# Optimization experiments

Measured on AMD Instinct MI355X. Metric: run time of the kernel, lower is better.

Reference implementation:

```python
import jax, jax.numpy as jnp
import numpy as np

NEG_INF = -1e30  # fp32-safe sentinel for masked max


def setup_inputs() -> dict:
    key = jax.random.key(0)
    ks = jax.random.split(key, 8)
    E = 65536          # num_edge
    S = 1              # neg_samples
    D = 200            # dim_in_time + dim_in_node
    H = 100            # hardcoded hidden width of src_fc/dst_fc
    T = 8              # num edge types
    C = 1              # predict_class
    scale = 1.0 / np.sqrt(D)
    return {
        "h": jax.random.normal(ks[0], (E * (S + 2), D), dtype=jnp.float32),
        "src_W": jax.random.normal(ks[1], (T, D, H), dtype=jnp.float32) * scale,
        "src_b": jax.random.normal(ks[2], (T, H), dtype=jnp.float32) * 0.01,
        "dst_W": jax.random.normal(ks[3], (T, D, H), dtype=jnp.float32) * scale,
        "dst_b": jax.random.normal(ks[4], (T, H), dtype=jnp.float32) * 0.01,
        "out_W": jax.random.normal(ks[5], (T, H, C), dtype=jnp.float32) * (1.0 / np.sqrt(H)),
        "out_b": jax.random.normal(ks[6], (T, C), dtype=jnp.float32) * 0.01,
        "poss_edgetypes": jax.random.randint(ks[7], (E * (1 + S), T), 0, 2, dtype=jnp.int32),
        "neg_samples": S,
    }


def _masked_max_pred(h_s, h_d, mask, src_W, src_b, dst_W, dst_b, out_W, out_b):
    # h_s, h_d: [N, D]; mask: [N, T] bool
    src_enc = jnp.einsum('nd,tdh->nth', h_s, src_W) + src_b      # [N, T, H]
    dst_enc = jnp.einsum('nd,tdh->nth', h_d, dst_W) + dst_b      # [N, T, H]
    hid = jax.nn.relu(src_enc + dst_enc)                          # [N, T, H]
    pred = jnp.einsum('nth,thc->ntc', hid, out_W) + out_b        # [N, T, C]
    masked = jnp.where(mask[:, :, None], pred, NEG_INF)
    best = jnp.max(masked, axis=1)                                # [N, C]
    any_valid = jnp.any(mask, axis=1, keepdims=True)
    return jnp.where(any_valid, best, 0.0)                        # zeros if no valid type


def reference(h, src_W, src_b, dst_W, dst_b, out_W, out_b, poss_edgetypes, neg_samples):
    E = h.shape[0] // (neg_samples + 2)
    h_src = h[:E]
    h_pos_dst = h[E:2 * E]
    h_neg_dst = h[2 * E:]                                         # [S*E, D], neg-major order
    mask = poss_edgetypes.astype(bool)
    pos_mask = mask[:E]
    neg_mask = mask[E:]
    pos_pred = _masked_max_pred(h_src, h_pos_dst, pos_mask,
                                src_W, src_b, dst_W, dst_b, out_W, out_b)
    h_src_tiled = jnp.tile(h_src, (neg_samples, 1))               # matches global_neg_idx = src + neg*E
    neg_pred = _masked_max_pred(h_src_tiled, h_neg_dst, neg_mask,
                                src_W, src_b, dst_W, dst_b, out_W, out_b)
    return pos_pred, neg_pred
```

## Files before the change

### kernel.cpp

```cpp
#include <hip/hip_runtime.h>
#include <stdint.h>


typedef float f32x4 __attribute__((ext_vector_type(4)));
typedef short s16x8 __attribute__((ext_vector_type(8)));

static constexpr int E_NODES  = 65536;
static constexpr int D_DIM    = 200;
static constexpr int H_DIM    = 100;
static constexpr int T_TYPES  = 8;
static constexpr int NPAD     = 112;
static constexpr int NT       = 7;
static constexpr int NSLAB    = 7;
static constexpr int P_TILE   = 128;
static constexpr int THREADS  = 256;
static constexpr int RS_TOTAL = T_TYPES * NSLAB;
static constexpr int SLAB_BYTES = NPAD * 64 * 2;
static constexpr int SLAB_XFERS = SLAB_BYTES / 16;

__device__ unsigned short g_Wt[RS_TOTAL * NPAD * 64];
__device__ float g_bias[T_TYPES * NPAD];
__device__ float g_outw[T_TYPES * NPAD];
__device__ float g_outb[T_TYPES];

__device__ __forceinline__ unsigned short f2bf(float f) {
  unsigned int u = __float_as_uint(f);
  u += 0x7FFFu + ((u >> 16) & 1u);
  return (unsigned short)(u >> 16);
}

__global__ void prep_weights(const float* __restrict__ srcW, const float* __restrict__ dstW,
                             const float* __restrict__ srcB, const float* __restrict__ dstB,
                             const float* __restrict__ outW, const float* __restrict__ outB) {
  int idx = blockIdx.x * blockDim.x + threadIdx.x;
  const int total = RS_TOTAL * NPAD * 64;
  if (idx < total) {
    int kk   = idx & 63;
    int j    = (idx >> 6) % NPAD;
    int rs   = (idx >> 6) / NPAD;
    int slab = rs % NSLAB;
    int t    = rs / NSLAB;
    int k    = slab * 64 + kk;
    float v = 0.0f;
    if (j < H_DIM) {
      if (k < D_DIM)                          v = srcW[(t * D_DIM + k) * H_DIM + j];
      else if (k >= 224 && k < 224 + D_DIM)   v = dstW[(t * D_DIM + (k - 224)) * H_DIM + j];
    }
    int kks = kk ^ ((j & 7) << 3);
    g_Wt[(rs * NPAD + j) * 64 + kks] = f2bf(v);
  }
  if (idx < T_TYPES * NPAD) {
    int t = idx / NPAD, j = idx % NPAD;
    float bb = 0.0f, ww = 0.0f;
    if (j < H_DIM) {
      bb = srcB[t * H_DIM + j] + dstB[t * H_DIM + j];
      ww = outW[t * H_DIM + j];
    }
    g_bias[idx] = bb;
    g_outw[idx] = ww;
    if (j == 0) g_outb[t] = outB[t];
  }
}

__device__ __forceinline__ void stage_B(int rs, unsigned short* dst, int tid) {
  char* src = (char*)g_Wt + (size_t)rs * SLAB_BYTES;
#pragma unroll
  for (int i = 0; i < 4; ++i) {
    int idx = i * THREADS + tid;
    if (idx < SLAB_XFERS) {
      __builtin_amdgcn_global_load_lds(
          (const __attribute__((address_space(1))) void*)(src + idx * 16),
          (__attribute__((address_space(3))) void*)(dst + idx * 8),
          16, 0, 0);
    }
  }
}

__global__ __launch_bounds__(THREADS, 2)
void fused_pred(const float* __restrict__ h, const int* __restrict__ poss,
                float* __restrict__ out) {
  __shared__ __align__(16) unsigned short ldsB[2][NPAD * 64];
  __shared__ __align__(16) int ldsMask[P_TILE * T_TYPES];

  const int tid  = threadIdx.x;
  const int lane = tid & 63;
  const int w    = tid >> 6;
  const int c    = lane & 15;
  const int g    = lane >> 4;
  const int P0   = (int)blockIdx.x * P_TILE;

  {
    const int4* mp = (const int4*)(poss + (size_t)P0 * T_TYPES);
    ((int4*)ldsMask)[tid] = mp[tid];
  }

  stage_B(0, ldsB[0], tid);

  s16x8 A[2][14];
#pragma unroll
  for (int mt = 0; mt < 2; ++mt) {
    const int row = w * 32 + mt * 16 + c;
    const int p   = P0 + row;
    const float* sp = h + (size_t)(p & (E_NODES - 1)) * D_DIM;
    const float* dp = h + ((size_t)E_NODES + (size_t)p) * D_DIM;
#pragma unroll
    for (int ks = 0; ks < 14; ++ks) {
      const float* base = (ks < 7) ? sp : dp;
      const int k0 = ((ks < 7) ? ks : (ks - 7)) * 32 + g * 8;
      s16x8 a = {};
      const bool valid = !((ks == 6 || ks == 13) && (g != 0));
      if (valid) {
        float4 f0 = *(const float4*)(base + k0);
        float4 f1 = *(const float4*)(base + k0 + 4);
        a[0] = (short)f2bf(f0.x); a[1] = (short)f2bf(f0.y);
        a[2] = (short)f2bf(f0.z); a[3] = (short)f2bf(f0.w);
        a[4] = (short)f2bf(f1.x); a[5] = (short)f2bf(f1.y);
        a[6] = (short)f2bf(f1.z); a[7] = (short)f2bf(f1.w);
      }
      A[mt][ks] = a;
    }
  }

  const f32x4 ZERO4 = {0.f, 0.f, 0.f, 0.f};
  f32x4 acc[2][NT];
#pragma unroll
  for (int mt = 0; mt < 2; ++mt)
#pragma unroll
    for (int nt = 0; nt < NT; ++nt) acc[mt][nt] = ZERO4;

  float runmax[2][4];
#pragma unroll
  for (int mt = 0; mt < 2; ++mt)
#pragma unroll
    for (int r = 0; r < 4; ++r) runmax[mt][r] = -1e30f;

  __syncthreads();

  int buf = 0;
  const int swz = (c & 7) << 4;
  for (int t = 0; t < T_TYPES; ++t) {
#pragma unroll
    for (int slab = 0; slab < NSLAB; ++slab) {
      const int s = t * NSLAB + slab;
      if (s + 1 < RS_TOTAL) stage_B(s + 1, ldsB[buf ^ 1], tid);

      const char* B = (const char*)ldsB[buf];
#pragma unroll
      for (int ksl = 0; ksl < 2; ++ksl) {
        const int koff = (ksl * 64 + g * 16) ^ swz;
        const s16x8 a0 = A[0][slab * 2 + ksl];
        const s16x8 a1 = A[1][slab * 2 + ksl];
#pragma unroll
        for (int nt = 0; nt < NT; ++nt) {
          s16x8 b = *(const s16x8*)(B + (nt * 16 + c) * 128 + koff);
          acc[0][nt] = __builtin_amdgcn_mfma_f32_16x16x32_bf16(a0, b, acc[0][nt], 0, 0, 0);
          acc[1][nt] = __builtin_amdgcn_mfma_f32_16x16x32_bf16(a1, b, acc[1][nt], 0, 0, 0);
        }
      }

      if (slab == NSLAB - 1) {
        float bj[NT], wj[NT];
#pragma unroll
        for (int nt = 0; nt < NT; ++nt) {
          const int j = t * NPAD + nt * 16 + c;
          bj[nt] = g_bias[j];
          wj[nt] = g_outw[j];
        }
        const float outb = g_outb[t];
#pragma unroll
        for (int mt = 0; mt < 2; ++mt) {
#pragma unroll
          for (int r = 0; r < 4; ++r) {
            float v = 0.f;
#pragma unroll
            for (int nt = 0; nt < NT; ++nt)
              v += fmaxf(acc[mt][nt][r] + bj[nt], 0.f) * wj[nt];
            v += __shfl_xor(v, 1);
            v += __shfl_xor(v, 2);
            v += __shfl_xor(v, 4);
            v += __shfl_xor(v, 8);
            const float pred = v + outb;
            const int row = w * 32 + mt * 16 + g * 4 + r;
            if (ldsMask[row * T_TYPES + t] != 0)
              runmax[mt][r] = fmaxf(runmax[mt][r], pred);
          }
#pragma unroll
          for (int nt = 0; nt < NT; ++nt) acc[mt][nt] = ZERO4;
        }
      }
      __syncthreads();
      buf ^= 1;
    }
  }

  if (c == 0) {
#pragma unroll
    for (int mt = 0; mt < 2; ++mt)
#pragma unroll
      for (int r = 0; r < 4; ++r) {
        const int row = w * 32 + mt * 16 + g * 4 + r;
        const float v = runmax[mt][r];
        out[P0 + row] = (v > -1e29f) ? v : 0.0f;
      }
  }
}

extern "C" void kernel_launch(void* const* d_in, const int* in_sizes, int n_in,
                              void* d_out, int out_size, void* d_ws, size_t ws_size,
                              hipStream_t stream) {
  const float* h    = (const float*)d_in[0];
  const float* srcW = (const float*)d_in[1];
  const float* srcB = (const float*)d_in[2];
  const float* dstW = (const float*)d_in[3];
  const float* dstB = (const float*)d_in[4];
  const float* outW = (const float*)d_in[5];
  const float* outB = (const float*)d_in[6];
  const int*   poss = (const int*)d_in[7];
  float* out = (float*)d_out;

  const int prep_total = RS_TOTAL * NPAD * 64;
  prep_weights<<<(prep_total + 255) / 256, 256, 0, stream>>>(srcW, dstW, srcB, dstB, outW, outB);

  const int nblocks = (2 * E_NODES) / P_TILE;
  fused_pred<<<nblocks, THREADS, 0, stream>>>(h, poss, out);
}
```

Baseline: 355.9 us.

## Pack K densely into 128-wide slabs, cut K-steps, remap blocks, stage bias in LDS

The weight layout packs the src and dst K ranges contiguously (400 instead of 448 padded), so each type needs 13 MFMA K-steps instead of 14. Weights are staged in 128-wide slabs, which halves the number of barrier-separated stages per type (4 instead of 7). Bias and output weights are now loaded into LDS inside the main kernel instead of a prep pass. The block index is remapped so that pos and neg tiles sharing the same src rows run close together, which should improve L2 reuse. LDS use per block roughly doubles for the B buffers, which may affect occupancy at 2 blocks per CU.

```diff
diff --git a/kernel.cpp b/kernel.cpp
--- a/kernel.cpp
+++ b/kernel.cpp
@@ -5,23 +5,22 @@
 typedef float f32x4 __attribute__((ext_vector_type(4)));
 typedef short s16x8 __attribute__((ext_vector_type(8)));
 
-static constexpr int E_NODES  = 65536;
-static constexpr int D_DIM    = 200;
-static constexpr int H_DIM    = 100;
-static constexpr int T_TYPES  = 8;
-static constexpr int NPAD     = 112;
-static constexpr int NT       = 7;
-static constexpr int NSLAB    = 7;
-static constexpr int P_TILE   = 128;
-static constexpr int THREADS  = 256;
-static constexpr int RS_TOTAL = T_TYPES * NSLAB;
-static constexpr int SLAB_BYTES = NPAD * 64 * 2;
-static constexpr int SLAB_XFERS = SLAB_BYTES / 16;
-
-__device__ unsigned short g_Wt[RS_TOTAL * NPAD * 64];
-__device__ float g_bias[T_TYPES * NPAD];
-__device__ float g_outw[T_TYPES * NPAD];
-__device__ float g_outb[T_TYPES];
+static constexpr int E_NODES = 65536;
+static constexpr int D_DIM   = 200;
+static constexpr int H_DIM   = 100;
+static constexpr int T_TYPES = 8;
+static constexpr int NPAD    = 112;
+static constexpr int NT      = 7;
+static constexpr int KS      = 13;
+static constexpr int BK      = 128;
+static constexpr int SLPT    = 4;
+static constexpr int P_TILE  = 128;
+static constexpr int THREADS = 256;
+static constexpr int N_INT   = T_TYPES * SLPT;
+static constexpr int SLAB_ELEMS = NPAD * BK;
+static constexpr int XFERS_PT   = SLAB_ELEMS * 2 / 16 / THREADS;
+
+__device__ unsigned short g_Wt[N_INT * SLAB_ELEMS];
 
 __device__ __forceinline__ unsigned short f2bf(float f) {
   unsigned int u = __float_as_uint(f);
@@ -29,74 +28,82 @@
   return (unsigned short)(u >> 16);
 }
 
-__global__ void prep_weights(const float* __restrict__ srcW, const float* __restrict__ dstW,
-                             const float* __restrict__ srcB, const float* __restrict__ dstB,
-                             const float* __restrict__ outW, const float* __restrict__ outB) {
+__global__ void prep_weights(const float* __restrict__ srcW, const float* __restrict__ dstW) {
   int idx = blockIdx.x * blockDim.x + threadIdx.x;
-  const int total = RS_TOTAL * NPAD * 64;
-  if (idx < total) {
-    int kk   = idx & 63;
-    int j    = (idx >> 6) % NPAD;
-    int rs   = (idx >> 6) / NPAD;
-    int slab = rs % NSLAB;
-    int t    = rs / NSLAB;
-    int k    = slab * 64 + kk;
-    float v = 0.0f;
-    if (j < H_DIM) {
-      if (k < D_DIM)                          v = srcW[(t * D_DIM + k) * H_DIM + j];
-      else if (k >= 224 && k < 224 + D_DIM)   v = dstW[(t * D_DIM + (k - 224)) * H_DIM + j];
-    }
-    int kks = kk ^ ((j & 7) << 3);
-    g_Wt[(rs * NPAD + j) * 64 + kks] = f2bf(v);
-  }
-  if (idx < T_TYPES * NPAD) {
-    int t = idx / NPAD, j = idx % NPAD;
-    float bb = 0.0f, ww = 0.0f;
-    if (j < H_DIM) {
-      bb = srcB[t * H_DIM + j] + dstB[t * H_DIM + j];
-      ww = outW[t * H_DIM + j];
-    }
-    g_bias[idx] = bb;
-    g_outw[idx] = ww;
-    if (j == 0) g_outb[t] = outB[t];
-  }
-}
-
-__device__ __forceinline__ void stage_B(int rs, unsigned short* dst, int tid) {
-  char* src = (char*)g_Wt + (size_t)rs * SLAB_BYTES;
-#pragma unroll
-  for (int i = 0; i < 4; ++i) {
-    int idx = i * THREADS + tid;
-    if (idx < SLAB_XFERS) {
-      __builtin_amdgcn_global_load_lds(
-          (const __attribute__((address_space(1))) void*)(src + idx * 16),
-          (__attribute__((address_space(3))) void*)(dst + idx * 8),
-          16, 0, 0);
-    }
+  const int total = N_INT * SLAB_ELEMS;
+  if (idx >= total) return;
+  int j   = idx % NPAD;
+  int rem = idx / NPAD;
+  int kk  = rem % BK;
+  int rs  = rem / BK;
+  int sl  = rs & 3;
+  int t   = rs >> 2;
+  int k   = sl * BK + kk;
+  float v = 0.0f;
+  if (j < H_DIM) {
+    if (k < D_DIM)            v = srcW[(t * D_DIM + k) * H_DIM + j];
+    else if (k < 2 * D_DIM)   v = dstW[(t * D_DIM + (k - D_DIM)) * H_DIM + j];
+  }
+  int kks = kk ^ ((j & 7) << 3);
+  g_Wt[(rs * NPAD + j) * BK + kks] = f2bf(v);
+}
+
+__device__ __forceinline__ void stage(int rs, unsigned short* dst, int tid) {
+  const char* src = (const char*)g_Wt + (size_t)rs * SLAB_ELEMS * 2;
+  char* d = (char*)dst;
+#pragma unroll
+  for (int i = 0; i < XFERS_PT; ++i) {
+    const int off = (i * THREADS + tid) * 16;
+    __builtin_amdgcn_global_load_lds(
+        (const __attribute__((address_space(1))) void*)(src + off),
+        (__attribute__((address_space(3))) void*)(d + off),
+        16, 0, 0);
   }
 }
 
 __global__ __launch_bounds__(THREADS, 2)
-void fused_pred(const float* __restrict__ h, const int* __restrict__ poss,
-                float* __restrict__ out) {
-  __shared__ __align__(16) unsigned short ldsB[2][NPAD * 64];
-  __shared__ __align__(16) int ldsMask[P_TILE * T_TYPES];
+void fused_pred(const float* __restrict__ h,
+                const float* __restrict__ srcB, const float* __restrict__ dstB,
+                const float* __restrict__ outW, const float* __restrict__ outB,
+                const int* __restrict__ poss, float* __restrict__ out) {
+  __shared__ __align__(16) unsigned short ldsB[2][SLAB_ELEMS];
+  __shared__ __align__(16) int   ldsMask[P_TILE * T_TYPES];
+  __shared__ float ldsBias[T_TYPES * NPAD];
+  __shared__ float ldsOutw[T_TYPES * NPAD];
+  __shared__ float ldsOutb[T_TYPES];
 
   const int tid  = threadIdx.x;
   const int lane = tid & 63;
   const int w    = tid >> 6;
   const int c    = lane & 15;
   const int g    = lane >> 4;
-  const int P0   = (int)blockIdx.x * P_TILE;
-
-  {
-    const int4* mp = (const int4*)(poss + (size_t)P0 * T_TYPES);
-    ((int4*)ldsMask)[tid] = mp[tid];
-  }
-
-  stage_B(0, ldsB[0], tid);
-
-  s16x8 A[2][14];
+
+  const int l     = ((int)blockIdx.x & 7) * 128 + ((int)blockIdx.x >> 3);
+  const int which = l & 1;
+  const int grp   = l >> 1;
+  const int P0    = which * E_NODES + grp * P_TILE;
+
+  stage(0, ldsB[0], tid);
+  __builtin_amdgcn_sched_barrier(0);
+
+#pragma unroll
+  for (int i = 0; i < 4; ++i) {
+    int idx = i * THREADS + tid;
+    if (idx < T_TYPES * NPAD) {
+      int t = idx / NPAD, j = idx - t * NPAD;
+      float bb = 0.f, ww = 0.f;
+      if (j < H_DIM) {
+        bb = srcB[t * H_DIM + j] + dstB[t * H_DIM + j];
+        ww = outW[t * H_DIM + j];
+      }
+      ldsBias[idx] = bb;
+      ldsOutw[idx] = ww;
+    }
+  }
+  if (tid < T_TYPES) ldsOutb[tid] = outB[tid];
+  ((int4*)ldsMask)[tid] = ((const int4*)(poss + (size_t)P0 * T_TYPES))[tid];
+
+  s16x8 A[2][KS];
 #pragma unroll
   for (int mt = 0; mt < 2; ++mt) {
     const int row = w * 32 + mt * 16 + c;
@@ -104,14 +111,13 @@
     const float* sp = h + (size_t)(p & (E_NODES - 1)) * D_DIM;
     const float* dp = h + ((size_t)E_NODES + (size_t)p) * D_DIM;
 #pragma unroll
-    for (int ks = 0; ks < 14; ++ks) {
-      const float* base = (ks < 7) ? sp : dp;
-      const int k0 = ((ks < 7) ? ks : (ks - 7)) * 32 + g * 8;
+    for (int ks = 0; ks < KS; ++ks) {
+      const int k0 = ks * 32 + g * 8;
       s16x8 a = {};
-      const bool valid = !((ks == 6 || ks == 13) && (g != 0));
-      if (valid) {
-        float4 f0 = *(const float4*)(base + k0);
-        float4 f1 = *(const float4*)(base + k0 + 4);
+      if (k0 < 2 * D_DIM) {
+        const float* base = (k0 < D_DIM) ? (sp + k0) : (dp + (k0 - D_DIM));
+        float4 f0 = *(const float4*)(base);
+        float4 f1 = *(const float4*)(base + 4);
         a[0] = (short)f2bf(f0.x); a[1] = (short)f2bf(f0.y);
         a[2] = (short)f2bf(f0.z); a[3] = (short)f2bf(f0.w);
         a[4] = (short)f2bf(f1.x); a[5] = (short)f2bf(f1.y);
@@ -123,50 +129,51 @@
 
   const f32x4 ZERO4 = {0.f, 0.f, 0.f, 0.f};
   f32x4 acc[2][NT];
-#pragma unroll
-  for (int mt = 0; mt < 2; ++mt)
+  float runmax[2][4];
+#pragma unroll
+  for (int mt = 0; mt < 2; ++mt) {
 #pragma unroll
     for (int nt = 0; nt < NT; ++nt) acc[mt][nt] = ZERO4;
-
-  float runmax[2][4];
-#pragma unroll
-  for (int mt = 0; mt < 2; ++mt)
 #pragma unroll
     for (int r = 0; r < 4; ++r) runmax[mt][r] = -1e30f;
+  }
+
+  const int swz = (c & 7) << 4;
 
   __syncthreads();
 
-  int buf = 0;
-  const int swz = (c & 7) << 4;
   for (int t = 0; t < T_TYPES; ++t) {
 #pragma unroll
-    for (int slab = 0; slab < NSLAB; ++slab) {
-      const int s = t * NSLAB + slab;
-      if (s + 1 < RS_TOTAL) stage_B(s + 1, ldsB[buf ^ 1], tid);
-
-      const char* B = (const char*)ldsB[buf];
-#pragma unroll
-      for (int ksl = 0; ksl < 2; ++ksl) {
-        const int koff = (ksl * 64 + g * 16) ^ swz;
-        const s16x8 a0 = A[0][slab * 2 + ksl];
-        const s16x8 a1 = A[1][slab * 2 + ksl];
+    for (int sl = 0; sl < SLPT; ++sl) {
+      if (sl < SLPT - 1 || t < T_TYPES - 1)
+        stage(t * SLPT + sl + 1, ldsB[(sl + 1) & 1], tid);
+      __builtin_amdgcn_sched_barrier(0);
+
+      const char* B = (const char*)ldsB[sl & 1];
+#pragma unroll
+      for (int ksl = 0; ksl < 4; ++ksl) {
+        const int ksg = sl * 4 + ksl;
+        if (ksg < KS) {
+          const int koff = (ksl * 64 + g * 16) ^ swz;
+          const s16x8 a0 = A[0][ksg];
+          const s16x8 a1 = A[1][ksg];
+#pragma unroll
+          for (int nt = 0; nt < NT; ++nt) {
+            s16x8 b = *(const s16x8*)(B + (nt * 16 + c) * 256 + koff);
+            acc[0][nt] = __builtin_amdgcn_mfma_f32_16x16x32_bf16(a0, b, acc[0][nt], 0, 0, 0);
+            acc[1][nt] = __builtin_amdgcn_mfma_f32_16x16x32_bf16(a1, b, acc[1][nt], 0, 0, 0);
+          }
+        }
+      }
+
+      if (sl == SLPT - 1) {
+        float bj[NT], wj[NT];
 #pragma unroll
         for (int nt = 0; nt < NT; ++nt) {
-          s16x8 b = *(const s16x8*)(B + (nt * 16 + c) * 128 + koff);
-          acc[0][nt] = __builtin_amdgcn_mfma_f32_16x16x32_bf16(a0, b, acc[0][nt], 0, 0, 0);
-          acc[1][nt] = __builtin_amdgcn_mfma_f32_16x16x32_bf16(a1, b, acc[1][nt], 0, 0, 0);
+          bj[nt] = ldsBias[t * NPAD + nt * 16 + c];
+          wj[nt] = ldsOutw[t * NPAD + nt * 16 + c];
         }
-      }
-
-      if (slab == NSLAB - 1) {
-        float bj[NT], wj[NT];
-#pragma unroll
-        for (int nt = 0; nt < NT; ++nt) {
-          const int j = t * NPAD + nt * 16 + c;
-          bj[nt] = g_bias[j];
-          wj[nt] = g_outw[j];
-        }
-        const float outb = g_outb[t];
+        const float ob = ldsOutb[t];
 #pragma unroll
         for (int mt = 0; mt < 2; ++mt) {
 #pragma unroll
@@ -179,7 +186,7 @@
             v += __shfl_xor(v, 2);
             v += __shfl_xor(v, 4);
             v += __shfl_xor(v, 8);
-            const float pred = v + outb;
+            const float pred = v + ob;
             const int row = w * 32 + mt * 16 + g * 4 + r;
             if (ldsMask[row * T_TYPES + t] != 0)
               runmax[mt][r] = fmaxf(runmax[mt][r], pred);
@@ -188,8 +195,8 @@
           for (int nt = 0; nt < NT; ++nt) acc[mt][nt] = ZERO4;
         }
       }
+
       __syncthreads();
-      buf ^= 1;
     }
   }
 
@@ -218,9 +225,9 @@
   const int*   poss = (const int*)d_in[7];
   float* out = (float*)d_out;
 
-  const int prep_total = RS_TOTAL * NPAD * 64;
-  prep_weights<<<(prep_total + 255) / 256, 256, 0, stream>>>(srcW, dstW, srcB, dstB, outW, outB);
+  const int prep_total = N_INT * SLAB_ELEMS;
+  prep_weights<<<(prep_total + 255) / 256, 256, 0, stream>>>(srcW, dstW);
 
   const int nblocks = (2 * E_NODES) / P_TILE;
-  fused_pred<<<nblocks, THREADS, 0, stream>>>(h, poss, out);
-}
+  fused_pred<<<nblocks, THREADS, 0, stream>>>(h, srcB, dstB, outW, outB, poss, out);
+}
```

Result: faster. 328.9 us (-7.6%).
